# Optimization experiments

Measured on AMD Instinct MI355X. Metric: run time of the kernel, lower is better.

The kernel has to match this reference:

```python
import jax, jax.numpy as jnp
import numpy as np

# Quantization / crossbar-simulation hyperparameters (from args)
WLA = 8          # wl_activate / wl_input bits
WLW = 8          # wl_weight bits
CELLBIT = 2      # bits stored per memory cell
ADC = 6          # ADC precision bits
SUB = 128        # crossbar subArray rows
ONOFF = 10.0     # cell on/off conductance ratio
STRIDE = 2
EPS = 1e-5


def _ste_round(v):
    return v + jax.lax.stop_gradient(jnp.round(v) - v)


def setup_inputs() -> dict:
    key = jax.random.key(0)
    ks = jax.random.split(key, 7)
    B, C, H, W, O = 16, 512, 28, 28, 1024
    x = jax.random.normal(ks[0], (B, C, H, W), dtype=jnp.float32)
    y = jax.random.normal(ks[1], (B, O, H // STRIDE, W // STRIDE), dtype=jnp.float32)
    bn_gamma = 1.0 + 0.1 * jax.random.normal(ks[2], (C,), dtype=jnp.float32)
    bn_beta = 0.1 * jax.random.normal(ks[3], (C,), dtype=jnp.float32)
    bn_mean = 0.1 * jax.random.normal(ks[4], (C,), dtype=jnp.float32)
    bn_var = jax.random.uniform(ks[5], (C,), dtype=jnp.float32, minval=0.5, maxval=1.5)
    w = 0.05 * jax.random.normal(ks[6], (O, C, 1, 1), dtype=jnp.float32)
    return {"x": x, "y": y, "bn_gamma": bn_gamma, "bn_beta": bn_beta,
            "bn_mean": bn_mean, "bn_var": bn_var, "w": w}


def _shortcut_q(x, y, bn_gamma, bn_beta, bn_mean, bn_var, w):
    # BatchNorm (inference, running stats) + ReLU
    inv = jax.lax.rsqrt(bn_var + EPS)
    xh = jax.nn.relu((x - bn_mean[None, :, None, None]) * (inv * bn_gamma)[None, :, None, None]
                     + bn_beta[None, :, None, None])

    aQ = float(2 ** WLA - 1)
    wQ = float(2 ** (WLW - 1) - 1)
    SHIFT = 2 ** (WLW - 1)  # map signed int weights to unsigned cells

    # Activation quantization to WLA unsigned bits (post-ReLU, per-tensor scale)
    a_max = jnp.maximum(jnp.max(xh), 1e-8)
    x_int = _ste_round(jnp.clip(xh / a_max, 0.0, 1.0) * aQ)          # [B,C,H,W] in [0, 255]
    xs = x_int[:, :, ::STRIDE, ::STRIDE]                              # 1x1 conv, stride 2

    # Weight quantization to WLW signed bits (per-tensor scale)
    w2 = w[:, :, 0, 0]                                                # [O,C]
    w_max = jnp.maximum(jnp.max(jnp.abs(w2)), 1e-8)
    w_int = _ste_round(jnp.clip(w2 / w_max, -1.0, 1.0) * wQ)          # [-127, 127]

    # Ideal integer conv (used for STE backward path)
    ideal = jnp.einsum('oc,bchw->bohw', w_int, xs)

    # --- analog crossbar simulation: bit-sliced inputs x cell-sliced weights + ADC ---
    cellRange = 2 ** CELLBIT
    nsl = WLW // CELLBIT
    off = (cellRange - 1) / (ONOFF - 1.0)                             # min-conductance offset
    B, C, Ho, Wo = xs.shape
    O = w2.shape[0]
    G = C // SUB                                                      # subarray groups along rows
    xg = xs.reshape(B, G, SUB, Ho, Wo)
    wu = (w_int + float(SHIFT)).reshape(O, G, SUB)                    # unsigned cell values
    vmax = SUB * (cellRange - 1 + off)                                # max per-column analog sum
    delta = vmax / float(2 ** ADC - 1)                                # ADC LSB

    sim = jnp.zeros_like(ideal)
    for z in range(WLA):                                              # input bit planes
        xb = jnp.floor(xg / (2.0 ** z)) % 2.0                         # [B,G,S,Ho,Wo] in {0,1}
        xsum = xb.sum(axis=2)                                         # dummy-column input [B,G,Ho,Wo]
        for k in range(nsl):                                          # weight cell slices
            wk = jnp.floor(wu / float(cellRange ** k)) % cellRange + off   # [O,G,S]
            dk = float((SHIFT // cellRange ** k) % cellRange) + off        # dummy cell value
            psum = jnp.einsum('ogs,bgshw->bgohw', wk, xb)             # analog column sums
            psum_q = jnp.round(psum / delta) * delta                  # ADC quantization
            dummy_q = jnp.round(dk * xsum / delta) * delta            # ADC on dummy column
            sim = sim + (2.0 ** z) * (float(cellRange) ** k) * (psum_q - dummy_q[:, :, None]).sum(axis=1)

    # STE: forward = simulated, backward = ideal quantized conv
    out_int = ideal + jax.lax.stop_gradient(sim - ideal)
    return out_int * (w_max / wQ) * (a_max / aQ) + y


def reference(x, y, bn_gamma, bn_beta, bn_mean, bn_var, w):
    return _shortcut_q(x, y, bn_gamma, bn_beta, bn_mean, bn_var, w)
```

## Files before the change

### kernel.cpp

```cpp
#include <hip/hip_runtime.h>
#include <math.h>

typedef __attribute__((ext_vector_type(4))) int i32x4;
typedef __attribute__((ext_vector_type(16))) int i32x16;

namespace {
constexpr int B_ = 16, C_ = 512, H_ = 28, W_ = 28, O_ = 1024;
constexpr int Ho_ = 14, Wo_ = 14;
constexpr int N_ = 3136, HW_ = 196;
constexpr int M_ = N_ * 8;
constexpr size_t FIN_OFF   = 0;
constexpr size_t AMAXP_OFF = 256;
constexpr size_t WMAXP_OFF = 4096;
constexpr size_t CHS_OFF   = 6144;
constexpr size_t DUM_OFF   = 8192;
constexpr size_t ACT_OFF   = 32768;
constexpr size_t WGT_OFF   = ACT_OFF + (size_t)M_ * 512;
}

__device__ __forceinline__ void gload(const char* g, char* l) {
  __builtin_amdgcn_global_load_lds(
      (const __attribute__((address_space(1))) char*)g,
      (__attribute__((address_space(3))) char*)l, 16, 0, 0);
}

__global__ __launch_bounds__(256) void prep1_kernel(
    const float* __restrict__ x, const float* __restrict__ w,
    const float* __restrict__ gamma, const float* __restrict__ beta,
    const float* __restrict__ mean, const float* __restrict__ var,
    float* __restrict__ amaxp, float* __restrict__ wmaxp, float* __restrict__ chs) {
#pragma clang fp contract(off)
  __shared__ float red[4];
  const int bx = blockIdx.x, tid = threadIdx.x;
  if (bx < 896) {
    int id = bx * 256 + tid;
    int row = id / 28;
    int seg = id - row * 28;
    int c = row & 511;
    const float4* p = (const float4*)(x + (size_t)row * 784 + seg * 28);
    float mn = 1e30f, mx = -1e30f;
#pragma unroll
    for (int i = 0; i < 7; ++i) {
      float4 v = p[i];
      mn = fminf(mn, fminf(fminf(v.x, v.y), fminf(v.z, v.w)));
      mx = fmaxf(mx, fmaxf(fmaxf(v.x, v.y), fmaxf(v.z, v.w)));
    }
    float vf = var[c] + 1e-5f;
    float sc = (float)(1.0 / sqrt((double)vf)) * gamma[c];
    float f1 = (mn - mean[c]) * sc + beta[c];
    float f2 = (mx - mean[c]) * sc + beta[c];
    float m = fmaxf(fmaxf(f1, f2), 0.f);
#pragma unroll
    for (int o = 32; o > 0; o >>= 1) m = fmaxf(m, __shfl_down(m, o, 64));
    if ((tid & 63) == 0) red[tid >> 6] = m;
    __syncthreads();
    if (tid == 0) amaxp[bx] = fmaxf(fmaxf(red[0], red[1]), fmaxf(red[2], red[3]));
  } else if (bx < 1152) {
    int id = (bx - 896) * 256 + tid;
    const float4* p = (const float4*)w + (size_t)id * 2;
    float4 v0 = p[0], v1 = p[1];
    float m = fmaxf(fmaxf(fmaxf(fabsf(v0.x), fabsf(v0.y)), fmaxf(fabsf(v0.z), fabsf(v0.w))),
                    fmaxf(fmaxf(fabsf(v1.x), fabsf(v1.y)), fmaxf(fabsf(v1.z), fabsf(v1.w))));
#pragma unroll
    for (int o = 32; o > 0; o >>= 1) m = fmaxf(m, __shfl_down(m, o, 64));
    if ((tid & 63) == 0) red[tid >> 6] = m;
    __syncthreads();
    if (tid == 0) wmaxp[bx - 896] = fmaxf(fmaxf(red[0], red[1]), fmaxf(red[2], red[3]));
  } else {
    int c = (bx - 1152) * 256 + tid;
    float vf = var[c] + 1e-5f;
    chs[c] = (float)(1.0 / sqrt((double)vf)) * gamma[c];
  }
}

__global__ __launch_bounds__(256) void pack_x_kernel(
    const float* __restrict__ x, const float* __restrict__ mean,
    const float* __restrict__ beta, const float* __restrict__ chs,
    const float* __restrict__ amaxp, unsigned* __restrict__ act,
    float* __restrict__ fin) {
#pragma clang fp contract(off)
  __shared__ float samax;
  __shared__ unsigned char sx[14 * 256];
  const int bx = blockIdx.x, tid = threadIdx.x;
  const int chalf = bx & 1;
  const int bh = bx >> 1;
  const int b = bh / 14, h2 = bh - b * 14;
  if (tid < 64) {
    float m = 0.f;
    for (int i = tid; i < 896; i += 64) m = fmaxf(m, amaxp[i]);
#pragma unroll
    for (int o = 32; o > 0; o >>= 1) m = fmaxf(m, __shfl_down(m, o, 64));
    if (tid == 0) {
      float a = fmaxf(m, 1e-8f);
      samax = a;
      if (bx == 0) fin[0] = a;
    }
  }
  __syncthreads();
  const float amax = samax;
  const int cbase = chalf * 256;
  for (int it = 0; it < 7; ++it) {
    int id = it * 256 + tid;
    int cl = id / 7, q = id - cl * 7;
    int c = cbase + cl;
    const float4 v = *(const float4*)(x + (size_t)(b * 512 + c) * 784 + h2 * 56 + q * 4);
    float sc = chs[c], mu = mean[c], be = beta[c];
    float f0 = fmaxf((v.x - mu) * sc + be, 0.f);
    int i0 = (int)rintf(fminf(fmaxf(f0 / amax, 0.f), 1.f) * 255.0f);
    float f2 = fmaxf((v.z - mu) * sc + be, 0.f);
    int i2 = (int)rintf(fminf(fmaxf(f2 / amax, 0.f), 1.f) * 255.0f);
    sx[(2 * q) * 256 + cl] = (unsigned char)i0;
    sx[(2 * q + 1) * 256 + cl] = (unsigned char)i2;
  }
  __syncthreads();
  const int nbase = b * 196 + h2 * 14;
  for (int it = 0; it < 4; ++it) {
    int id = it * 256 + tid;
    if (id < 896) {
      int cql = id & 63, w2 = id >> 6;
      unsigned v = *(const unsigned*)(sx + w2 * 256 + cql * 4);
      int n = nbase + w2;
      int cq = chalf * 64 + cql;
#pragma unroll
      for (int z = 0; z < 8; ++z)
        act[(size_t)(n * 8 + z) * 128 + cq] = (v >> z) & 0x01010101u;
    }
  }
}

__global__ __launch_bounds__(256) void pack_wd_kernel(
    const float* __restrict__ w, const float* __restrict__ wmaxp,
    const unsigned char* __restrict__ act, unsigned* __restrict__ wgt,
    int* __restrict__ dummy, float* __restrict__ fin) {
#pragma clang fp contract(off)
  const int bx = blockIdx.x, tid = threadIdx.x;
  if (bx < 512) {
    __shared__ float swmax;
    if (tid < 64) {
      float m = fmaxf(fmaxf(wmaxp[tid], wmaxp[tid + 64]),
                      fmaxf(wmaxp[tid + 128], wmaxp[tid + 192]));
#pragma unroll
      for (int o = 32; o > 0; o >>= 1) m = fmaxf(m, __shfl_down(m, o, 64));
      if (tid == 0) {
        float a = fmaxf(m, 1e-8f);
        swmax = a;
        if (bx == 0) fin[1] = a;
      }
    }
    __syncthreads();
    const float wmax = swmax;
    int t = bx * 256 + tid;
    int c16 = t & 31, k = (t >> 5) & 3, o = t >> 7;
    unsigned words[4];
#pragma unroll
    for (int q = 0; q < 4; ++q) {
      unsigned wd = 0;
#pragma unroll
      for (int j = 0; j < 4; ++j) {
        int c = c16 * 16 + q * 4 + j;
        float v = fminf(fmaxf(w[(size_t)o * 512 + c] / wmax, -1.f), 1.f);
        int wi = (int)rintf(v * 127.0f);
        unsigned wu = (unsigned)(wi + 128);
        unsigned cell = (wu >> (2 * k)) & 3u;
        wd |= (3u * cell + 1u) << (8 * j);
      }
      words[q] = wd;
    }
    *(uint4*)(wgt + ((size_t)(o * 4 + k) * 512 + c16 * 16) / 4) =
        make_uint4(words[0], words[1], words[2], words[3]);
  } else {
    int id = (bx - 512) * 256 + tid;
    int g = id & 3, z = (id >> 2) & 7, n = id >> 5;
    const uint4* a = (const uint4*)(act + (size_t)(n * 8 + z) * 512 + g * 128);
    int xs = 0;
#pragma unroll
    for (int t8 = 0; t8 < 8; ++t8) {
      uint4 v = a[t8];
      xs += __popc(v.x) + __popc(v.y) + __popc(v.z) + __popc(v.w);
    }
    unsigned q0 = (__umul24((unsigned)xs, 51610u) + 524288u) >> 20;
    unsigned q3 = (__umul24((unsigned)xs, 361268u) + 524288u) >> 20;
    int term = (int)((__umul24(q0, 21u) + (q3 << 6)) << z);
#pragma unroll
    for (int msk = 1; msk <= 16; msk <<= 1) term += __shfl_xor(term, msk, 64);
    if ((tid & 31) == 0) dummy[n] = term;
  }
}

#define STAGEB(s_, p_) {                                  \
  char* lb = lds + (p_) * 16384 + ldst;                   \
  gload(gB + (s_) * 128 +  0, lb);                        \
  gload(gB + (s_) * 128 + 32, lb + 4096);                 \
  gload(gB + (s_) * 128 + 64, lb + 8192);                 \
  gload(gB + (s_) * 128 + 96, lb + 12288);                \
}

#define APREF(s_, p_) {                                   \
  ar[p_][0] = *(const i32x4*)(gA + (s_) * 128 +  0);      \
  ar[p_][1] = *(const i32x4*)(gA + (s_) * 128 + 32);      \
  ar[p_][2] = *(const i32x4*)(gA + (s_) * 128 + 64);      \
  ar[p_][3] = *(const i32x4*)(gA + (s_) * 128 + 96);      \
}

#define CPASS(pb_, p_, cp0_) {                                        \
  i32x16 c0, c1;                                                      \
  _Pragma("unroll")                                                   \
  for (int e = 0; e < 16; ++e) { c0[e] = 0; c1[e] = 0; }              \
  _Pragma("unroll")                                                   \
  for (int j = 0; j < 4; ++j) {                                       \
    i32x4 b0 = *(const i32x4*)(rB + (pb_) + j * 4096 + (cp0_) * 512); \
    i32x4 b1 = *(const i32x4*)(rB + (pb_) + j * 4096 + (cp0_) * 512 + 512); \
    c0 = __builtin_amdgcn_mfma_i32_32x32x32_i8(ar[p_][j], b0, c0, 0, 0, 0); \
    c1 = __builtin_amdgcn_mfma_i32_32x32x32_i8(ar[p_][j], b1, c1, 0, 0, 0); \
  }                                                                   \
  _Pragma("unroll")                                                   \
  for (int e = 0; e < 16; ++e) {                                      \
    unsigned q0q = (__umul24((unsigned)c0[e], 51610u) + 524288u) >> 20; \
    acc[(cp0_)][e >> 2] += (int)(q0q << shr[e & 3]);                  \
    unsigned q1q = (__umul24((unsigned)c1[e], 51610u) + 524288u) >> 20; \
    acc[(cp0_) + 1][e >> 2] += (int)(q1q << shr[e & 3]);              \
  }                                                                   \
}

#define COMPUTE(pb_, p_) { CPASS(pb_, p_, 0) CPASS(pb_, p_, 2) }

__global__ __launch_bounds__(256, 4) void shortcutq_main_kernel(
    const char* __restrict__ act, const char* __restrict__ wgt,
    const int* __restrict__ dummy, const float* __restrict__ y,
    const float* __restrict__ fin, float* __restrict__ out) {
  __shared__ __align__(16) char lds[32768];
  const int tid = threadIdx.x;
  const int cblk = blockIdx.x;
  const int mblk = blockIdx.y;
  const int lane = tid & 63, wv = tid >> 6;

  const char* gA = act + (size_t)(mblk * 128 + wv * 32 + (lane & 31)) * 512 +
                   (lane >> 5) * 16;
  const char* gB = wgt + (size_t)(cblk * 128 + (tid & 127)) * 512 + (tid >> 7) * 16;
  const int ldst = tid * 16;

  const char* rB = lds + (lane >> 5) * 2048 + (lane & 31) * 16;

  const int shb = 4 * (lane >> 5) + 2 * (lane & 3);
  int shr[4] = {shb, shb + 1, shb + 2, shb + 3};

  i32x4 ar[2][4];
  int acc[4][4];
#pragma unroll
  for (int i = 0; i < 4; ++i)
#pragma unroll
    for (int j = 0; j < 4; ++j) acc[i][j] = 0;

  APREF(0, 0)
  STAGEB(0, 0)
  __syncthreads();
  APREF(1, 1)
  STAGEB(1, 1)
  COMPUTE(0, 0)
  __syncthreads();
  APREF(2, 0)
  STAGEB(2, 0)
  COMPUTE(16384, 1)
  __syncthreads();
  APREF(3, 1)
  STAGEB(3, 1)
  COMPUTE(0, 0)
  __syncthreads();
  COMPUTE(16384, 1)

  const float scale = (float)((128.0 * (3.0 + 1.0 / 3.0)) / 63.0) *
                      (fin[1] / 127.0f) * (fin[0] / 255.0f);
  int sums[4][4];
#pragma unroll
  for (int cp = 0; cp < 4; ++cp)
#pragma unroll
    for (int cc = 0; cc < 4; ++cc) {
      int v = acc[cp][cc];
      v += __shfl_xor(v, 1, 64);
      v += __shfl_xor(v, 2, 64);
      v += __shfl_xor(v, 32, 64);
      sums[cp][cc] = v;
    }
  if ((lane & 3) == 0 && lane < 32) {
    const int ol = lane >> 2;
#pragma unroll
    for (int cc = 0; cc < 4; ++cc) {
      int n = mblk * 16 + wv * 4 + cc;
      int d = dummy[n];
      int b = n / 196, hw = n - b * 196;
#pragma unroll
      for (int cp = 0; cp < 4; ++cp) {
        int o = cblk * 32 + cp * 8 + ol;
        size_t idx = ((size_t)(b * 1024 + o)) * 196 + hw;
        out[idx] = (float)(sums[cp][cc] - d) * scale + y[idx];
      }
    }
  }
}

extern "C" void kernel_launch(void* const* d_in, const int* in_sizes, int n_in,
                              void* d_out, int out_size, void* d_ws, size_t ws_size,
                              hipStream_t stream) {
  const float* x     = (const float*)d_in[0];
  const float* y     = (const float*)d_in[1];
  const float* gamma = (const float*)d_in[2];
  const float* beta  = (const float*)d_in[3];
  const float* mean  = (const float*)d_in[4];
  const float* var   = (const float*)d_in[5];
  const float* w     = (const float*)d_in[6];
  float* out = (float*)d_out;

  char* wsb = (char*)d_ws;
  float* fin    = (float*)(wsb + FIN_OFF);
  float* amaxp  = (float*)(wsb + AMAXP_OFF);
  float* wmaxp  = (float*)(wsb + WMAXP_OFF);
  float* chs    = (float*)(wsb + CHS_OFF);
  int*   dum    = (int*)(wsb + DUM_OFF);
  char*  actb   = wsb + ACT_OFF;
  char*  wgtb   = wsb + WGT_OFF;

  hipLaunchKernelGGL(prep1_kernel, dim3(1154), dim3(256), 0, stream,
                     x, w, gamma, beta, mean, var, amaxp, wmaxp, chs);
  hipLaunchKernelGGL(pack_x_kernel, dim3(448), dim3(256), 0, stream,
                     x, mean, beta, chs, amaxp, (unsigned*)actb, fin);
  hipLaunchKernelGGL(pack_wd_kernel, dim3(904), dim3(256), 0, stream,
                     w, wmaxp, (const unsigned char*)actb, (unsigned*)wgtb, dum, fin);
  hipLaunchKernelGGL(shortcutq_main_kernel, dim3(32, 196), dim3(256), 0, stream,
                     actb, wgtb, dum, y, fin, out);
}
```

Before: 215.1 us.

## Fuse dummy-column computation into GEMM and merge packing kernels

Removes the separate dummy-column popcount pass and computes the per-row dummy term inside the main MFMA kernel from the already-loaded activation bit planes, summing bytes with SWAR adds and shuffles. The x and w packing kernels are merged into one launch, and the main kernel's wave tiling changes to a 2x2 split so each wave reuses one B fragment across two A fragments. This saves a kernel launch, a re-read of the activation buffer and the dummy buffer traffic. In exchange it adds some integer work and register pressure to the main kernel.

```diff
diff --git a/kernel.cpp b/kernel.cpp
--- a/kernel.cpp
+++ b/kernel.cpp
@@ -5,15 +5,12 @@
 typedef __attribute__((ext_vector_type(16))) int i32x16;
 
 namespace {
-constexpr int B_ = 16, C_ = 512, H_ = 28, W_ = 28, O_ = 1024;
-constexpr int Ho_ = 14, Wo_ = 14;
-constexpr int N_ = 3136, HW_ = 196;
+constexpr int N_ = 3136;
 constexpr int M_ = N_ * 8;
 constexpr size_t FIN_OFF   = 0;
 constexpr size_t AMAXP_OFF = 256;
 constexpr size_t WMAXP_OFF = 4096;
 constexpr size_t CHS_OFF   = 6144;
-constexpr size_t DUM_OFF   = 8192;
 constexpr size_t ACT_OFF   = 32768;
 constexpr size_t WGT_OFF   = ACT_OFF + (size_t)M_ * 512;
 }
@@ -73,69 +70,64 @@
   }
 }
 
-__global__ __launch_bounds__(256) void pack_x_kernel(
+__global__ __launch_bounds__(256) void pack_xw_kernel(
     const float* __restrict__ x, const float* __restrict__ mean,
     const float* __restrict__ beta, const float* __restrict__ chs,
-    const float* __restrict__ amaxp, unsigned* __restrict__ act,
-    float* __restrict__ fin) {
-#pragma clang fp contract(off)
-  __shared__ float samax;
-  __shared__ unsigned char sx[14 * 256];
-  const int bx = blockIdx.x, tid = threadIdx.x;
-  const int chalf = bx & 1;
-  const int bh = bx >> 1;
-  const int b = bh / 14, h2 = bh - b * 14;
-  if (tid < 64) {
-    float m = 0.f;
-    for (int i = tid; i < 896; i += 64) m = fmaxf(m, amaxp[i]);
-#pragma unroll
-    for (int o = 32; o > 0; o >>= 1) m = fmaxf(m, __shfl_down(m, o, 64));
-    if (tid == 0) {
-      float a = fmaxf(m, 1e-8f);
-      samax = a;
-      if (bx == 0) fin[0] = a;
-    }
-  }
-  __syncthreads();
-  const float amax = samax;
-  const int cbase = chalf * 256;
-  for (int it = 0; it < 7; ++it) {
-    int id = it * 256 + tid;
-    int cl = id / 7, q = id - cl * 7;
-    int c = cbase + cl;
-    const float4 v = *(const float4*)(x + (size_t)(b * 512 + c) * 784 + h2 * 56 + q * 4);
-    float sc = chs[c], mu = mean[c], be = beta[c];
-    float f0 = fmaxf((v.x - mu) * sc + be, 0.f);
-    int i0 = (int)rintf(fminf(fmaxf(f0 / amax, 0.f), 1.f) * 255.0f);
-    float f2 = fmaxf((v.z - mu) * sc + be, 0.f);
-    int i2 = (int)rintf(fminf(fmaxf(f2 / amax, 0.f), 1.f) * 255.0f);
-    sx[(2 * q) * 256 + cl] = (unsigned char)i0;
-    sx[(2 * q + 1) * 256 + cl] = (unsigned char)i2;
-  }
-  __syncthreads();
-  const int nbase = b * 196 + h2 * 14;
-  for (int it = 0; it < 4; ++it) {
-    int id = it * 256 + tid;
-    if (id < 896) {
-      int cql = id & 63, w2 = id >> 6;
-      unsigned v = *(const unsigned*)(sx + w2 * 256 + cql * 4);
-      int n = nbase + w2;
-      int cq = chalf * 64 + cql;
-#pragma unroll
-      for (int z = 0; z < 8; ++z)
-        act[(size_t)(n * 8 + z) * 128 + cq] = (v >> z) & 0x01010101u;
-    }
-  }
-}
-
-__global__ __launch_bounds__(256) void pack_wd_kernel(
-    const float* __restrict__ w, const float* __restrict__ wmaxp,
-    const unsigned char* __restrict__ act, unsigned* __restrict__ wgt,
-    int* __restrict__ dummy, float* __restrict__ fin) {
+    const float* __restrict__ amaxp, const float* __restrict__ w,
+    const float* __restrict__ wmaxp, unsigned* __restrict__ act,
+    unsigned* __restrict__ wgt, float* __restrict__ fin) {
 #pragma clang fp contract(off)
   const int bx = blockIdx.x, tid = threadIdx.x;
-  if (bx < 512) {
+  if (bx < 448) {
+    __shared__ float samax;
+    __shared__ unsigned char sx[14 * 256];
+    const int chalf = bx & 1;
+    const int bh = bx >> 1;
+    const int b = bh / 14, h2 = bh - b * 14;
+    if (tid < 64) {
+      float m = 0.f;
+      for (int i = tid; i < 896; i += 64) m = fmaxf(m, amaxp[i]);
+#pragma unroll
+      for (int o = 32; o > 0; o >>= 1) m = fmaxf(m, __shfl_down(m, o, 64));
+      if (tid == 0) {
+        float a = fmaxf(m, 1e-8f);
+        samax = a;
+        if (bx == 0) fin[0] = a;
+      }
+    }
+    __syncthreads();
+    const float amax = samax;
+    const int cbase = chalf * 256;
+    for (int it = 0; it < 7; ++it) {
+      int id = it * 256 + tid;
+      int cl = id / 7, q = id - cl * 7;
+      int c = cbase + cl;
+      const float4 v = *(const float4*)(x + (size_t)(b * 512 + c) * 784 + h2 * 56 + q * 4);
+      float sc = chs[c], mu = mean[c], be = beta[c];
+      float f0 = fmaxf((v.x - mu) * sc + be, 0.f);
+      int i0 = (int)rintf(fminf(fmaxf(f0 / amax, 0.f), 1.f) * 255.0f);
+      float f2 = fmaxf((v.z - mu) * sc + be, 0.f);
+      int i2 = (int)rintf(fminf(fmaxf(f2 / amax, 0.f), 1.f) * 255.0f);
+      sx[(2 * q) * 256 + cl] = (unsigned char)i0;
+      sx[(2 * q + 1) * 256 + cl] = (unsigned char)i2;
+    }
+    __syncthreads();
+    const int nbase = b * 196 + h2 * 14;
+    for (int it = 0; it < 4; ++it) {
+      int id = it * 256 + tid;
+      if (id < 896) {
+        int cql = id & 63, w2 = id >> 6;
+        unsigned v = *(const unsigned*)(sx + w2 * 256 + cql * 4);
+        int n = nbase + w2;
+        int cq = chalf * 64 + cql;
+#pragma unroll
+        for (int z = 0; z < 8; ++z)
+          act[(size_t)(n * 8 + z) * 128 + cq] = (v >> z) & 0x01010101u;
+      }
+    }
+  } else {
     __shared__ float swmax;
+    const int bx2 = bx - 448;
     if (tid < 64) {
       float m = fmaxf(fmaxf(wmaxp[tid], wmaxp[tid + 64]),
                       fmaxf(wmaxp[tid + 128], wmaxp[tid + 192]));
@@ -144,12 +136,12 @@
       if (tid == 0) {
         float a = fmaxf(m, 1e-8f);
         swmax = a;
-        if (bx == 0) fin[1] = a;
+        if (bx2 == 0) fin[1] = a;
       }
     }
     __syncthreads();
     const float wmax = swmax;
-    int t = bx * 256 + tid;
+    int t = bx2 * 256 + tid;
     int c16 = t & 31, k = (t >> 5) & 3, o = t >> 7;
     unsigned words[4];
 #pragma unroll
@@ -168,22 +160,6 @@
     }
     *(uint4*)(wgt + ((size_t)(o * 4 + k) * 512 + c16 * 16) / 4) =
         make_uint4(words[0], words[1], words[2], words[3]);
-  } else {
-    int id = (bx - 512) * 256 + tid;
-    int g = id & 3, z = (id >> 2) & 7, n = id >> 5;
-    const uint4* a = (const uint4*)(act + (size_t)(n * 8 + z) * 512 + g * 128);
-    int xs = 0;
-#pragma unroll
-    for (int t8 = 0; t8 < 8; ++t8) {
-      uint4 v = a[t8];
-      xs += __popc(v.x) + __popc(v.y) + __popc(v.z) + __popc(v.w);
-    }
-    unsigned q0 = (__umul24((unsigned)xs, 51610u) + 524288u) >> 20;
-    unsigned q3 = (__umul24((unsigned)xs, 361268u) + 524288u) >> 20;
-    int term = (int)((__umul24(q0, 21u) + (q3 << 6)) << z);
-#pragma unroll
-    for (int msk = 1; msk <= 16; msk <<= 1) term += __shfl_xor(term, msk, 64);
-    if ((tid & 31) == 0) dummy[n] = term;
   }
 }
 
@@ -195,106 +171,135 @@
   gload(gB + (s_) * 128 + 96, lb + 12288);                \
 }
 
-#define APREF(s_, p_) {                                   \
-  ar[p_][0] = *(const i32x4*)(gA + (s_) * 128 +  0);      \
-  ar[p_][1] = *(const i32x4*)(gA + (s_) * 128 + 32);      \
-  ar[p_][2] = *(const i32x4*)(gA + (s_) * 128 + 64);      \
-  ar[p_][3] = *(const i32x4*)(gA + (s_) * 128 + 96);      \
-}
-
-#define CPASS(pb_, p_, cp0_) {                                        \
-  i32x16 c0, c1;                                                      \
-  _Pragma("unroll")                                                   \
-  for (int e = 0; e < 16; ++e) { c0[e] = 0; c1[e] = 0; }              \
-  _Pragma("unroll")                                                   \
-  for (int j = 0; j < 4; ++j) {                                       \
-    i32x4 b0 = *(const i32x4*)(rB + (pb_) + j * 4096 + (cp0_) * 512); \
-    i32x4 b1 = *(const i32x4*)(rB + (pb_) + j * 4096 + (cp0_) * 512 + 512); \
-    c0 = __builtin_amdgcn_mfma_i32_32x32x32_i8(ar[p_][j], b0, c0, 0, 0, 0); \
-    c1 = __builtin_amdgcn_mfma_i32_32x32x32_i8(ar[p_][j], b1, c1, 0, 0, 0); \
-  }                                                                   \
-  _Pragma("unroll")                                                   \
-  for (int e = 0; e < 16; ++e) {                                      \
-    unsigned q0q = (__umul24((unsigned)c0[e], 51610u) + 524288u) >> 20; \
-    acc[(cp0_)][e >> 2] += (int)(q0q << shr[e & 3]);                  \
-    unsigned q1q = (__umul24((unsigned)c1[e], 51610u) + 524288u) >> 20; \
-    acc[(cp0_) + 1][e >> 2] += (int)(q1q << shr[e & 3]);              \
-  }                                                                   \
-}
-
-#define COMPUTE(pb_, p_) { CPASS(pb_, p_, 0) CPASS(pb_, p_, 2) }
+#define CSPASS(pb_, cs_) {                                                  \
+  i32x16 c0, c1;                                                            \
+  _Pragma("unroll")                                                         \
+  for (int e = 0; e < 16; ++e) { c0[e] = 0; c1[e] = 0; }                    \
+  _Pragma("unroll")                                                         \
+  for (int j = 0; j < 4; ++j) {                                             \
+    i32x4 bf = *(const i32x4*)(rB + (pb_) + j * 4096 + (cs_) * 512);        \
+    c0 = __builtin_amdgcn_mfma_i32_32x32x32_i8(av[0][j], bf, c0, 0, 0, 0);  \
+    c1 = __builtin_amdgcn_mfma_i32_32x32x32_i8(av[1][j], bf, c1, 0, 0, 0);  \
+  }                                                                         \
+  _Pragma("unroll")                                                         \
+  for (int e = 0; e < 16; ++e) {                                            \
+    unsigned q0q = (__umul24((unsigned)c0[e], 51610u) + 524288u) >> 20;     \
+    acc[0][cs_][e >> 2] += (int)(q0q << shr[e & 3]);                        \
+    unsigned q1q = (__umul24((unsigned)c1[e], 51610u) + 524288u) >> 20;     \
+    acc[1][cs_][e >> 2] += (int)(q1q << shr[e & 3]);                        \
+  }                                                                         \
+}
+
+#define STAGE_BODY(s_, p_, pref_) {                                         \
+  i32x4 av[2][4];                                                           \
+  _Pragma("unroll")                                                         \
+  for (int s2 = 0; s2 < 2; ++s2)                                            \
+    _Pragma("unroll")                                                       \
+    for (int j = 0; j < 4; ++j)                                             \
+      av[s2][j] = *(const i32x4*)(gA + s2 * 16384 + (s_) * 128 + j * 32);   \
+  if (pref_) { STAGEB((s_) + 1, 1 - (p_)) }                                 \
+  unsigned xsh[2];                                                          \
+  _Pragma("unroll")                                                         \
+  for (int s2 = 0; s2 < 2; ++s2) {                                          \
+    unsigned bs = 0;                                                        \
+    _Pragma("unroll")                                                       \
+    for (int j = 0; j < 4; ++j)                                             \
+      bs += (unsigned)av[s2][j].x + (unsigned)av[s2][j].y +                 \
+            (unsigned)av[s2][j].z + (unsigned)av[s2][j].w;                  \
+    unsigned t = (bs & 0x00FF00FFu) + ((bs >> 8) & 0x00FF00FFu);            \
+    xsh[s2] = (t & 0xFFFFu) + (t >> 16);                                    \
+  }                                                                         \
+  _Pragma("unroll")                                                         \
+  for (int s2 = 0; s2 < 2; ++s2) {                                          \
+    unsigned xsf = xsh[s2] + (unsigned)__shfl_xor((int)xsh[s2], 32, 64);    \
+    unsigned q0 = (__umul24(xsf, 51610u) + 524288u) >> 20;                  \
+    unsigned q3 = (__umul24(xsf, 361268u) + 524288u) >> 20;                 \
+    dacc[s2] += (int)((__umul24(q0, 21u) + (q3 << 6)) << zz);               \
+  }                                                                         \
+  const int pb_ = (p_) * 16384;                                             \
+  CSPASS(pb_, 0) CSPASS(pb_, 1)                                             \
+}
 
 __global__ __launch_bounds__(256, 4) void shortcutq_main_kernel(
     const char* __restrict__ act, const char* __restrict__ wgt,
-    const int* __restrict__ dummy, const float* __restrict__ y,
-    const float* __restrict__ fin, float* __restrict__ out) {
+    const float* __restrict__ y, const float* __restrict__ fin,
+    float* __restrict__ out) {
   __shared__ __align__(16) char lds[32768];
   const int tid = threadIdx.x;
   const int cblk = blockIdx.x;
   const int mblk = blockIdx.y;
   const int lane = tid & 63, wv = tid >> 6;
-
-  const char* gA = act + (size_t)(mblk * 128 + wv * 32 + (lane & 31)) * 512 +
+  const int wm = wv >> 1, wn = wv & 1;
+
+  const char* gA = act + (size_t)(mblk * 128 + wm * 64 + (lane & 31)) * 512 +
                    (lane >> 5) * 16;
   const char* gB = wgt + (size_t)(cblk * 128 + (tid & 127)) * 512 + (tid >> 7) * 16;
   const int ldst = tid * 16;
-
-  const char* rB = lds + (lane >> 5) * 2048 + (lane & 31) * 16;
+  const char* rB = lds + (lane >> 5) * 2048 + wn * 1024 + (lane & 31) * 16;
 
   const int shb = 4 * (lane >> 5) + 2 * (lane & 3);
   int shr[4] = {shb, shb + 1, shb + 2, shb + 3};
-
-  i32x4 ar[2][4];
-  int acc[4][4];
-#pragma unroll
-  for (int i = 0; i < 4; ++i)
-#pragma unroll
-    for (int j = 0; j < 4; ++j) acc[i][j] = 0;
-
-  APREF(0, 0)
+  const int zz = lane & 7;
+
+  int acc[2][2][4];
+#pragma unroll
+  for (int i = 0; i < 2; ++i)
+#pragma unroll
+    for (int j = 0; j < 2; ++j)
+#pragma unroll
+      for (int cc = 0; cc < 4; ++cc) acc[i][j][cc] = 0;
+  int dacc[2] = {0, 0};
+
   STAGEB(0, 0)
   __syncthreads();
-  APREF(1, 1)
-  STAGEB(1, 1)
-  COMPUTE(0, 0)
+  STAGE_BODY(0, 0, 1)
   __syncthreads();
-  APREF(2, 0)
-  STAGEB(2, 0)
-  COMPUTE(16384, 1)
+  STAGE_BODY(1, 1, 1)
   __syncthreads();
-  APREF(3, 1)
-  STAGEB(3, 1)
-  COMPUTE(0, 0)
+  STAGE_BODY(2, 0, 1)
   __syncthreads();
-  COMPUTE(16384, 1)
+  STAGE_BODY(3, 1, 0)
 
   const float scale = (float)((128.0 * (3.0 + 1.0 / 3.0)) / 63.0) *
                       (fin[1] / 127.0f) * (fin[0] / 255.0f);
-  int sums[4][4];
-#pragma unroll
-  for (int cp = 0; cp < 4; ++cp)
-#pragma unroll
-    for (int cc = 0; cc < 4; ++cc) {
-      int v = acc[cp][cc];
-      v += __shfl_xor(v, 1, 64);
-      v += __shfl_xor(v, 2, 64);
-      v += __shfl_xor(v, 32, 64);
-      sums[cp][cc] = v;
-    }
+  int sums[2][2][4];
+#pragma unroll
+  for (int s2 = 0; s2 < 2; ++s2)
+#pragma unroll
+    for (int cs = 0; cs < 2; ++cs)
+#pragma unroll
+      for (int cc = 0; cc < 4; ++cc) {
+        int v = acc[s2][cs][cc];
+        v += __shfl_xor(v, 1, 64);
+        v += __shfl_xor(v, 2, 64);
+        v += __shfl_xor(v, 32, 64);
+        sums[s2][cs][cc] = v;
+      }
+  int dn[2][4];
+#pragma unroll
+  for (int s2 = 0; s2 < 2; ++s2) {
+    int v = dacc[s2];
+    v += __shfl_xor(v, 1, 64);
+    v += __shfl_xor(v, 2, 64);
+    v += __shfl_xor(v, 4, 64);
+#pragma unroll
+    for (int cc = 0; cc < 4; ++cc) dn[s2][cc] = __shfl(v, cc * 8, 64);
+  }
   if ((lane & 3) == 0 && lane < 32) {
     const int ol = lane >> 2;
 #pragma unroll
-    for (int cc = 0; cc < 4; ++cc) {
-      int n = mblk * 16 + wv * 4 + cc;
-      int d = dummy[n];
-      int b = n / 196, hw = n - b * 196;
-#pragma unroll
-      for (int cp = 0; cp < 4; ++cp) {
-        int o = cblk * 32 + cp * 8 + ol;
-        size_t idx = ((size_t)(b * 1024 + o)) * 196 + hw;
-        out[idx] = (float)(sums[cp][cc] - d) * scale + y[idx];
-      }
-    }
+    for (int s2 = 0; s2 < 2; ++s2)
+#pragma unroll
+      for (int cc = 0; cc < 4; ++cc) {
+        int n = mblk * 16 + wm * 8 + s2 * 4 + cc;
+        int b = n / 196, hw = n - b * 196;
+#pragma unroll
+        for (int cs = 0; cs < 2; ++cs) {
+          int o = cblk * 32 + (wn * 2 + cs) * 8 + ol;
+          size_t idx = ((size_t)(b * 1024 + o)) * 196 + hw;
+          out[idx] = (float)(sums[s2][cs][cc] - dn[s2][cc]) * scale + y[idx];
+        }
+      }
   }
 }
 
@@ -315,16 +320,14 @@
   float* amaxp  = (float*)(wsb + AMAXP_OFF);
   float* wmaxp  = (float*)(wsb + WMAXP_OFF);
   float* chs    = (float*)(wsb + CHS_OFF);
-  int*   dum    = (int*)(wsb + DUM_OFF);
   char*  actb   = wsb + ACT_OFF;
   char*  wgtb   = wsb + WGT_OFF;
 
   hipLaunchKernelGGL(prep1_kernel, dim3(1154), dim3(256), 0, stream,
                      x, w, gamma, beta, mean, var, amaxp, wmaxp, chs);
-  hipLaunchKernelGGL(pack_x_kernel, dim3(448), dim3(256), 0, stream,
-                     x, mean, beta, chs, amaxp, (unsigned*)actb, fin);
-  hipLaunchKernelGGL(pack_wd_kernel, dim3(904), dim3(256), 0, stream,
-                     w, wmaxp, (const unsigned char*)actb, (unsigned*)wgtb, dum, fin);
+  hipLaunchKernelGGL(pack_xw_kernel, dim3(960), dim3(256), 0, stream,
+                     x, mean, beta, chs, amaxp, w, wmaxp,
+                     (unsigned*)actb, (unsigned*)wgtb, fin);
   hipLaunchKernelGGL(shortcutq_main_kernel, dim3(32, 196), dim3(256), 0, stream,
-                     actb, wgtb, dum, y, fin, out);
-}
+                     actb, wgtb, y, fin, out);
+}
```

Measured after the change: 250.5 us. 1.16x slower.
